# Kernel optimization log

Measured on AMD Instinct MI355X. Metric: run time of the kernel, lower is better.

Reference implementation:

```python
import jax, jax.numpy as jnp
import numpy as np

N, E, D = 100_000, 1_250_000, 64
EPS = 1e-8

def setup_inputs() -> dict:
    key = jax.random.key(0)
    ks = jax.random.split(key, 8)
    h = jax.random.normal(ks[0], (N, D), jnp.float32)
    eig = jax.random.normal(ks[1], (E, 1), jnp.float32)          # per-edge vector field
    snorm_n = jax.random.uniform(ks[2], (N, 1), jnp.float32)     # node norm
    src = jax.random.randint(ks[3], (E,), 0, N)
    dst = jax.random.randint(ks[4], (E,), 0, N)
    # pretrans: Linear(2D -> D); posttrans: Linear((3+1)*D -> D); torch Linear weight is [out, in]
    W1 = jax.random.normal(ks[5], (D, 2 * D), jnp.float32) / np.sqrt(2.0 * D)
    b1 = jnp.zeros((D,), jnp.float32)
    W2 = jax.random.normal(ks[6], (D, 4 * D), jnp.float32) / np.sqrt(4.0 * D)
    b2 = jnp.zeros((D,), jnp.float32)
    gamma = jnp.ones((D,), jnp.float32)   # BatchNorm1d weight
    beta = jnp.zeros((D,), jnp.float32)   # BatchNorm1d bias
    return dict(h=h, eig=eig, snorm_n=snorm_n, src=src, dst=dst,
                W1=W1, b1=b1, W2=W2, b2=b2, gamma=gamma, beta=beta)

def reference(h, eig, snorm_n, src, dst, W1, b1, W2, b2, gamma, beta):
    seg = lambda x: jax.ops.segment_sum(x, dst, num_segments=N)
    # pretrans on edges: MLP(cat[h_src, h_dst])
    z2 = jnp.concatenate([h[src], h[dst]], axis=1)   # [E, 2D]
    e = z2 @ W1.T + b1                                # [E, D]
    deg = seg(jnp.ones((E, 1), e.dtype))              # [N, 1]
    # aggregator: mean
    agg_mean = seg(e) / jnp.maximum(deg, 1.0)
    # aggregator: max (empty segments -> 0)
    agg_max = jax.ops.segment_max(e, dst, num_segments=N)
    agg_max = jnp.where(deg > 0, agg_max, 0.0)
    # aggregator: directional derivative dir_dx
    absum = seg(jnp.abs(eig))                         # [N, 1] sum of |vf| per node
    w = eig / (absum[dst] + EPS)                      # [E, 1] normalized weights
    agg_dir = jnp.abs(seg(e * w) - seg(w) * h)        # [N, D]
    # posttrans on nodes
    hc = jnp.concatenate([h, agg_mean, agg_max, agg_dir], axis=1)  # [N, 4D]
    h2 = (hc @ W2.T + b2) * snorm_n
    # BatchNorm1d (training mode: batch stats, biased variance)
    mu = jnp.mean(h2, axis=0)
    var = jnp.var(h2, axis=0)
    h2 = (h2 - mu) * jax.lax.rsqrt(var + 1e-5) * gamma + beta
    h2 = jax.nn.relu(h2)
    # residual (in_dim == out_dim); dropout p=0 is identity
    return h + h2
```

## Files before the change

### kernel.cpp

```cpp
#include <hip/hip_runtime.h>
#include <math.h>

__device__ __forceinline__ float bf2f(unsigned short s) {
    return __uint_as_float(((unsigned)s) << 16);
}
__device__ __forceinline__ unsigned short f2bf(float f) {
    unsigned u = __float_as_uint(f);
    unsigned r = (u + 0x7fffu + ((u >> 16) & 1u)) >> 16;
    return (unsigned short)r;
}

typedef __attribute__((ext_vector_type(8))) short short8v;
typedef __attribute__((ext_vector_type(4))) float f32x4;

__global__ __launch_bounds__(256) void edge_rank_kernel(
    const int* __restrict__ dst, int* __restrict__ cursor, int* __restrict__ rank, int E)
{
    int e = blockIdx.x * 256 + threadIdx.x;
    if (e < E) {
        rank[e] = atomicAdd(&cursor[dst[e]], 1);
    }
}

__global__ __launch_bounds__(256) void block_reduce_kernel(
    const int* __restrict__ deg, int* __restrict__ bsum, int N)
{
    __shared__ int sd[256];
    int t = threadIdx.x;
    int i = blockIdx.x * 256 + t;
    sd[t] = (i < N) ? deg[i] : 0;
    __syncthreads();
    for (int s = 128; s > 0; s >>= 1) {
        if (t < s) sd[t] += sd[t + s];
        __syncthreads();
    }
    if (t == 0) bsum[blockIdx.x] = sd[0];
}

__global__ __launch_bounds__(1024) void scan_bsums_kernel(
    const int* __restrict__ bsum, int* __restrict__ bscan, int nb)
{
    __shared__ int sd[1024];
    int t = threadIdx.x;
    int own = (t < nb) ? bsum[t] : 0;
    sd[t] = own;
    __syncthreads();
    for (int off = 1; off < 1024; off <<= 1) {
        int v = (t >= off) ? sd[t - off] : 0;
        __syncthreads();
        sd[t] += v;
        __syncthreads();
    }
    if (t < nb) bscan[t] = sd[t] - own;
}

__global__ __launch_bounds__(256) void block_scan_kernel(
    const int* __restrict__ deg, const int* __restrict__ bscan,
    int* __restrict__ offs, int N)
{
    __shared__ int sd[256];
    int t = threadIdx.x;
    int i = blockIdx.x * 256 + t;
    int myv = (i < N) ? deg[i] : 0;
    sd[t] = myv;
    __syncthreads();
    for (int off = 1; off < 256; off <<= 1) {
        int v = (t >= off) ? sd[t - off] : 0;
        __syncthreads();
        sd[t] += v;
        __syncthreads();
    }
    if (i < N) {
        offs[i] = sd[t] - myv + bscan[blockIdx.x];
    }
}

__global__ __launch_bounds__(256) void csr_scatter_kernel(
    const int* __restrict__ src, const int* __restrict__ dst, const float* __restrict__ eig,
    const int* __restrict__ rank, const int* __restrict__ offs,
    int2* __restrict__ csr, int E)
{
    int e = blockIdx.x * 256 + threadIdx.x;
    if (e < E) {
        int dn = dst[e];
        int p = offs[dn] + rank[e];
        csr[p] = make_int2(src[e], __float_as_int(eig[e]));
    }
}

__global__ __launch_bounds__(256) void uv_kernel(
    const float* __restrict__ h, const float* __restrict__ W1, const float* __restrict__ b1,
    unsigned short* __restrict__ u, unsigned short* __restrict__ v,
    unsigned short* __restrict__ hb, int N)
{
    __shared__ float wT[64 * 128];
    __shared__ float hs[64 * 68];
    int t = threadIdx.x;
    for (int idx = t; idx < 64 * 128; idx += 256) {
        int j = idx >> 7, c = idx & 127;
        int d = c & 63;
        int col = (c < 64) ? j : (64 + j);
        wT[idx] = W1[d * 128 + col];
    }
    int n0 = blockIdx.x * 64;
    for (int r = 0; r < 16; ++r) {
        int idx = r * 256 + t;
        int nl = idx >> 6, j = idx & 63;
        int n = n0 + nl;
        hs[nl * 68 + j] = (n < N) ? h[(size_t)n * 64 + j] : 0.f;
    }
    __syncthreads();

    for (int it = 0; it < 2; ++it) {
        int idx = it * 256 + t;
        int nl = idx >> 3, j8 = idx & 7;
        int n = n0 + nl;
        if (n < N) {
            union { unsigned short s[8]; uint4 v4; } pk;
#pragma unroll
            for (int m = 0; m < 8; ++m) pk.s[m] = f2bf(hs[nl * 68 + j8 * 8 + m]);
            *(uint4*)(hb + (size_t)n * 64 + j8 * 8) = pk.v4;
        }
    }

    int nb = (t & 15) * 4;
    int cb = (t >> 4) * 8;
    float acc[4][8];
#pragma unroll
    for (int i = 0; i < 4; ++i)
#pragma unroll
        for (int k = 0; k < 8; ++k) acc[i][k] = 0.f;

    for (int j = 0; j < 64; ++j) {
        float wv[8];
#pragma unroll
        for (int k = 0; k < 8; ++k) wv[k] = wT[j * 128 + cb + k];
#pragma unroll
        for (int i = 0; i < 4; ++i) {
            float hv = hs[(nb + i) * 68 + j];
#pragma unroll
            for (int k = 0; k < 8; ++k) acc[i][k] = fmaf(hv, wv[k], acc[i][k]);
        }
    }

    bool isV = (cb >= 64);
    int dbase = cb & 63;
#pragma unroll
    for (int i = 0; i < 4; ++i) {
        int n = n0 + nb + i;
        if (n < N) {
            union { unsigned short s[8]; uint4 v4; } pk;
            if (!isV) {
#pragma unroll
                for (int k = 0; k < 8; ++k) pk.s[k] = f2bf(acc[i][k]);
                *(uint4*)(u + (size_t)n * 64 + dbase) = pk.v4;
            } else {
#pragma unroll
                for (int k = 0; k < 8; ++k) pk.s[k] = f2bf(acc[i][k] + b1[dbase + k]);
                *(uint4*)(v + (size_t)n * 64 + dbase) = pk.v4;
            }
        }
    }
}

__global__ __launch_bounds__(256) void w2bf_kernel(
    const float* __restrict__ W2, unsigned short* __restrict__ w2bf)
{
    int idx = blockIdx.x * 256 + threadIdx.x;
    if (idx < 64 * 256) w2bf[idx] = f2bf(W2[idx]);
}

__global__ __launch_bounds__(256) void agg_kernel(
    const unsigned short* __restrict__ u, const unsigned short* __restrict__ v,
    const float* __restrict__ h,
    const int* __restrict__ offs, const int* __restrict__ degi,
    const int2* __restrict__ csr,
    unsigned short* __restrict__ agg, int N)
{
    int gw = (blockIdx.x * 256 + threadIdx.x) >> 6;
    int lane = threadIdx.x & 63;
    int n = __builtin_amdgcn_readfirstlane(gw);
    if (n >= N) return;
    int beg = offs[n];
    int dn = degi[n];

    float accs = 0.f, accd = 0.f, accm = -3.402823466e38f;
    float pa = 0.f, ps = 0.f;
    for (int i0 = 0; i0 < dn; i0 += 64) {
        int cnt = min(dn - i0, 64);
        int idxv = 0; float wvv = 0.f;
        if (lane < cnt) {
            int2 rec = csr[beg + i0 + lane];
            idxv = rec.x;
            wvv = __int_as_float(rec.y);
        }
        pa += fabsf(wvv);
        ps += wvv;
        int j = 0;
        for (; j + 4 <= cnt; j += 4) {
            int s0 = __shfl(idxv, j), s1 = __shfl(idxv, j + 1);
            int s2 = __shfl(idxv, j + 2), s3 = __shfl(idxv, j + 3);
            float w0 = __shfl(wvv, j), w1 = __shfl(wvv, j + 1);
            float w2_ = __shfl(wvv, j + 2), w3 = __shfl(wvv, j + 3);
            float u0 = bf2f(u[(size_t)s0 * 64 + lane]);
            float u1 = bf2f(u[(size_t)s1 * 64 + lane]);
            float u2 = bf2f(u[(size_t)s2 * 64 + lane]);
            float u3 = bf2f(u[(size_t)s3 * 64 + lane]);
            accs += (u0 + u1) + (u2 + u3);
            accm = fmaxf(accm, fmaxf(fmaxf(u0, u1), fmaxf(u2, u3)));
            accd = fmaf(w0, u0, fmaf(w1, u1, fmaf(w2_, u2, fmaf(w3, u3, accd))));
        }
        for (; j < cnt; ++j) {
            int s0 = __shfl(idxv, j);
            float w0 = __shfl(wvv, j);
            float u0 = bf2f(u[(size_t)s0 * 64 + lane]);
            accs += u0;
            accm = fmaxf(accm, u0);
            accd = fmaf(w0, u0, accd);
        }
    }
#pragma unroll
    for (int w = 1; w < 64; w <<= 1) {
        pa += __shfl_xor(pa, w);
        ps += __shfl_xor(ps, w);
    }
    float inv_ab = 1.f / (pa + 1e-8f);
    float segw = ps * inv_ab;

    float vl = bf2f(v[(size_t)n * 64 + lane]);
    float hl = h[(size_t)n * 64 + lane];
    float fdeg = (float)dn;
    float mean = (accs + fdeg * vl) / fmaxf(fdeg, 1.f);
    float amax = (dn > 0) ? (accm + vl) : 0.f;
    float adir = fabsf(fmaf(accd, inv_ab, segw * (vl - hl)));
    size_t base = (size_t)n * 192;
    agg[base + lane]       = f2bf(mean);
    agg[base + 64 + lane]  = f2bf(amax);
    agg[base + 128 + lane] = f2bf(adir);
}

__global__ __launch_bounds__(256) void post_mfma_kernel(
    const unsigned short* __restrict__ hb, const unsigned short* __restrict__ agg,
    const unsigned short* __restrict__ w2bf, const float* __restrict__ b2,
    const float* __restrict__ snorm, float* __restrict__ h2,
    float* __restrict__ bn_buf, int N)
{
    int lane = threadIdx.x & 63;
    int w = threadIdx.x >> 6;
    int lr = lane & 15;
    int lg = lane >> 4;

    short8v a[8];
    {
        const unsigned short* ab = w2bf + ((size_t)(w * 16 + lr)) * 256 + lg * 8;
#pragma unroll
        for (int s = 0; s < 8; ++s)
            a[s] = *(const short8v*)(ab + s * 32);
    }
    float4 b2v = *(const float4*)(b2 + w * 16 + lg * 4);
    float b2a[4] = {b2v.x, b2v.y, b2v.z, b2v.w};

    int n0 = blockIdx.x * 256;
    float s1[4] = {0.f, 0.f, 0.f, 0.f}, s2[4] = {0.f, 0.f, 0.f, 0.f};

#pragma unroll 2
    for (int t = 0; t < 16; ++t) {
        int node = n0 + t * 16 + lr;
        bool ok = node < N;
        short8v b[8];
        if (ok) {
            const unsigned short* hbp = hb  + (size_t)node * 64  + lg * 8;
            const unsigned short* agp = agg + (size_t)node * 192 + lg * 8;
            b[0] = *(const short8v*)(hbp);
            b[1] = *(const short8v*)(hbp + 32);
#pragma unroll
            for (int s = 2; s < 8; ++s)
                b[s] = *(const short8v*)(agp + (s - 2) * 32);
        } else {
#pragma unroll
            for (int s = 0; s < 8; ++s) b[s] = (short8v)0;
        }
        f32x4 acc0 = {0.f, 0.f, 0.f, 0.f}, acc1 = {0.f, 0.f, 0.f, 0.f};
#pragma unroll
        for (int s = 0; s < 8; s += 2) {
            acc0 = __builtin_amdgcn_mfma_f32_16x16x32_bf16(a[s],     b[s],     acc0, 0, 0, 0);
            acc1 = __builtin_amdgcn_mfma_f32_16x16x32_bf16(a[s + 1], b[s + 1], acc1, 0, 0, 0);
        }
        float sn = ok ? snorm[node] : 0.f;
        float xr[4];
#pragma unroll
        for (int r = 0; r < 4; ++r) {
            xr[r] = (acc0[r] + acc1[r] + b2a[r]) * sn;
            s1[r] += xr[r];
            s2[r] = fmaf(xr[r], xr[r], s2[r]);
        }
        if (ok) {
            *(float4*)(h2 + (size_t)node * 64 + w * 16 + lg * 4) =
                make_float4(xr[0], xr[1], xr[2], xr[3]);
        }
    }

#pragma unroll
    for (int m = 1; m < 16; m <<= 1) {
#pragma unroll
        for (int r = 0; r < 4; ++r) {
            s1[r] += __shfl_xor(s1[r], m);
            s2[r] += __shfl_xor(s2[r], m);
        }
    }
    if (lr == 0) {
        int d = w * 16 + lg * 4;
#pragma unroll
        for (int r = 0; r < 4; ++r) {
            atomicAdd(&bn_buf[d + r], s1[r]);
            atomicAdd(&bn_buf[64 + d + r], s2[r]);
        }
    }
}

__global__ __launch_bounds__(256) void bn_final_kernel(
    const float* __restrict__ h, const float* __restrict__ h2,
    const float* __restrict__ bn_buf, const float* __restrict__ gamma,
    const float* __restrict__ beta, float* __restrict__ out, int N, float invN)
{
    int idx = blockIdx.x * 256 + threadIdx.x;
    int total4 = N * 16;
    if (idx >= total4) return;
    int base = idx * 4;
    int d0 = base & 63;
    const float4 a = *(const float4*)(h2 + base);
    const float4 hh = *(const float4*)(h + base);
    float r[4] = {a.x, a.y, a.z, a.w};
    float hv[4] = {hh.x, hh.y, hh.z, hh.w};
    float o[4];
#pragma unroll
    for (int k = 0; k < 4; ++k) {
        int d = d0 + k;
        float mu = bn_buf[d] * invN;
        float var = bn_buf[64 + d] * invN - mu * mu;
        float rstd = rsqrtf(var + 1e-5f);
        float x = (r[k] - mu) * rstd * gamma[d] + beta[d];
        o[k] = hv[k] + fmaxf(x, 0.f);
    }
    float4 ov = {o[0], o[1], o[2], o[3]};
    *(float4*)(out + base) = ov;
}

extern "C" void kernel_launch(void* const* d_in, const int* in_sizes, int n_in,
                              void* d_out, int out_size, void* d_ws, size_t ws_size,
                              hipStream_t stream)
{
    const float* h     = (const float*)d_in[0];
    const float* eig   = (const float*)d_in[1];
    const float* snorm = (const float*)d_in[2];
    const int*   src   = (const int*)d_in[3];
    const int*   dst   = (const int*)d_in[4];
    const float* W1    = (const float*)d_in[5];
    const float* b1    = (const float*)d_in[6];
    const float* W2    = (const float*)d_in[7];
    const float* b2    = (const float*)d_in[8];
    const float* gamma = (const float*)d_in[9];
    const float* beta  = (const float*)d_in[10];
    float* out = (float*)d_out;

    const int N = in_sizes[2];
    const int E = in_sizes[1];

    char* w = (char*)d_ws;
    size_t off = 0;
    auto alloc = [&](size_t bytes) -> char* {
        char* p = w + off;
        off += (bytes + 255) & ~size_t(255);
        return p;
    };
    unsigned short* u = (unsigned short*)alloc((size_t)N * 64 * 2);
    unsigned short* v = (unsigned short*)alloc((size_t)N * 64 * 2);
    float* h2 = (float*)u;
    unsigned short* agg = (unsigned short*)alloc((size_t)N * 192 * 2);
    unsigned short* hb  = (unsigned short*)alloc((size_t)N * 64 * 2);
    int2* csr = (int2*)alloc((size_t)E * 8);
    int*  rank = (int*)alloc((size_t)E * 4);
    char* zero_base = w + off;
    int*   cursor = (int*)alloc((size_t)N * 4);
    float* bn_buf = (float*)alloc(128 * 4);
    size_t zero_bytes = (size_t)((char*)(bn_buf + 128) - zero_base);
    int* offs = (int*)alloc((size_t)N * 4);
    int nb = (N + 255) / 256;
    int* bsum  = (int*)alloc((size_t)nb * 4);
    int* bscan = (int*)alloc((size_t)nb * 4);
    unsigned short* w2bf = (unsigned short*)alloc(64 * 256 * 2);
    (void)ws_size; (void)n_in; (void)out_size;

    hipMemsetAsync(zero_base, 0, zero_bytes, stream);

    int egrid = (E + 255) / 256;
    edge_rank_kernel<<<egrid, 256, 0, stream>>>(dst, cursor, rank, E);
    block_reduce_kernel<<<nb, 256, 0, stream>>>(cursor, bsum, N);
    scan_bsums_kernel<<<1, 1024, 0, stream>>>(bsum, bscan, nb);
    block_scan_kernel<<<nb, 256, 0, stream>>>(cursor, bscan, offs, N);
    csr_scatter_kernel<<<egrid, 256, 0, stream>>>(src, dst, eig, rank, offs, csr, E);

    int ntiles = (N + 63) / 64;
    uv_kernel<<<ntiles, 256, 0, stream>>>(h, W1, b1, u, v, hb, N);
    w2bf_kernel<<<64, 256, 0, stream>>>(W2, w2bf);

    int agrid = ((size_t)N * 64 + 255) / 256;
    agg_kernel<<<agrid, 256, 0, stream>>>(u, v, h, offs, cursor, csr, agg, N);

    post_mfma_kernel<<<(N + 255) / 256, 256, 0, stream>>>(hb, agg, w2bf, b2, snorm,
                                                          h2, bn_buf, N);

    int fgrid = (N * 16 + 255) / 256;
    bn_final_kernel<<<fgrid, 256, 0, stream>>>(h, h2, bn_buf, gamma, beta, out, N, 1.0f / (float)N);
}
```

Measured before the change: 374.6 us.

## Move pretrans node projection to bf16 MFMA and shrink post-MLP tiles

The scalar FP32 shared-memory GEMM that computes per-node u/v projections is replaced by a bf16 MFMA kernel reading a pre-cast bf16 copy of h and a pre-transposed bf16 W1. The h cast and weight conversion move into separate elementwise kernels, and the W1/W2 conversions are merged into one launch. The post-MLP MFMA kernel now handles 64 nodes per block instead of 256, giving four times as many blocks for better occupancy. The trade-off is an extra launch and an extra pass over h, plus u/v computed from bf16-rounded h rather than fp32 h.

Result: slower. 435.1 us (+16.1%).

```diff
diff --git a/kernel.cpp b/kernel.cpp
--- a/kernel.cpp
+++ b/kernel.cpp
@@ -88,86 +88,94 @@
     }
 }
 
-__global__ __launch_bounds__(256) void uv_kernel(
-    const float* __restrict__ h, const float* __restrict__ W1, const float* __restrict__ b1,
-    unsigned short* __restrict__ u, unsigned short* __restrict__ v,
-    unsigned short* __restrict__ hb, int N)
-{
-    __shared__ float wT[64 * 128];
-    __shared__ float hs[64 * 68];
-    int t = threadIdx.x;
-    for (int idx = t; idx < 64 * 128; idx += 256) {
-        int j = idx >> 7, c = idx & 127;
-        int d = c & 63;
-        int col = (c < 64) ? j : (64 + j);
-        wT[idx] = W1[d * 128 + col];
-    }
+__global__ __launch_bounds__(256) void hb_cast_kernel(
+    const float* __restrict__ h, unsigned short* __restrict__ hb, long total8)
+{
+    long idx = (long)blockIdx.x * 256 + threadIdx.x;
+    if (idx >= total8) return;
+    const float4 a = *(const float4*)(h + idx * 8);
+    const float4 b = *(const float4*)(h + idx * 8 + 4);
+    union { unsigned short s[8]; uint4 v4; } pk;
+    pk.s[0] = f2bf(a.x); pk.s[1] = f2bf(a.y); pk.s[2] = f2bf(a.z); pk.s[3] = f2bf(a.w);
+    pk.s[4] = f2bf(b.x); pk.s[5] = f2bf(b.y); pk.s[6] = f2bf(b.z); pk.s[7] = f2bf(b.w);
+    *(uint4*)(hb + idx * 8) = pk.v4;
+}
+
+__global__ __launch_bounds__(256) void wprep_kernel(
+    const float* __restrict__ W1, const float* __restrict__ W2,
+    unsigned short* __restrict__ w1bf, unsigned short* __restrict__ w2bf)
+{
+    int idx = blockIdx.x * 256 + threadIdx.x;
+    if (idx < 128 * 64) {
+        int c = idx >> 6, j = idx & 63;
+        float val = (c < 64) ? W1[c * 128 + j] : W1[(c - 64) * 128 + 64 + j];
+        w1bf[idx] = f2bf(val);
+    } else if (idx < 128 * 64 + 64 * 256) {
+        int k = idx - 128 * 64;
+        w2bf[k] = f2bf(W2[k]);
+    }
+}
+
+__global__ __launch_bounds__(256) void uv_mfma_kernel(
+    const unsigned short* __restrict__ hb, const unsigned short* __restrict__ w1bf,
+    const float* __restrict__ b1,
+    unsigned short* __restrict__ u, unsigned short* __restrict__ v, int N)
+{
+    int lane = threadIdx.x & 63;
+    int wv = threadIdx.x >> 6;
+    int lr = lane & 15;
+    int lg = lane >> 4;
+
+    short8v a[2][2];
+#pragma unroll
+    for (int rt = 0; rt < 2; ++rt)
+#pragma unroll
+        for (int s = 0; s < 2; ++s)
+            a[rt][s] = *(const short8v*)(w1bf + (size_t)(wv * 32 + rt * 16 + lr) * 64 + s * 32 + lg * 8);
+
+    float b1v[2][4];
+#pragma unroll
+    for (int rt = 0; rt < 2; ++rt) {
+        if (wv >= 2) {
+            float4 t4 = *(const float4*)(b1 + (wv - 2) * 32 + rt * 16 + lg * 4);
+            b1v[rt][0] = t4.x; b1v[rt][1] = t4.y; b1v[rt][2] = t4.z; b1v[rt][3] = t4.w;
+        } else {
+            b1v[rt][0] = b1v[rt][1] = b1v[rt][2] = b1v[rt][3] = 0.f;
+        }
+    }
+
+    unsigned short* outp = (wv < 2) ? u : v;
+    int coff0 = (wv & 1) * 32 + lg * 4;
+
     int n0 = blockIdx.x * 64;
-    for (int r = 0; r < 16; ++r) {
-        int idx = r * 256 + t;
-        int nl = idx >> 6, j = idx & 63;
-        int n = n0 + nl;
-        hs[nl * 68 + j] = (n < N) ? h[(size_t)n * 64 + j] : 0.f;
-    }
-    __syncthreads();
-
-    for (int it = 0; it < 2; ++it) {
-        int idx = it * 256 + t;
-        int nl = idx >> 3, j8 = idx & 7;
-        int n = n0 + nl;
-        if (n < N) {
-            union { unsigned short s[8]; uint4 v4; } pk;
-#pragma unroll
-            for (int m = 0; m < 8; ++m) pk.s[m] = f2bf(hs[nl * 68 + j8 * 8 + m]);
-            *(uint4*)(hb + (size_t)n * 64 + j8 * 8) = pk.v4;
-        }
-    }
-
-    int nb = (t & 15) * 4;
-    int cb = (t >> 4) * 8;
-    float acc[4][8];
-#pragma unroll
-    for (int i = 0; i < 4; ++i)
-#pragma unroll
-        for (int k = 0; k < 8; ++k) acc[i][k] = 0.f;
-
-    for (int j = 0; j < 64; ++j) {
-        float wv[8];
-#pragma unroll
-        for (int k = 0; k < 8; ++k) wv[k] = wT[j * 128 + cb + k];
-#pragma unroll
-        for (int i = 0; i < 4; ++i) {
-            float hv = hs[(nb + i) * 68 + j];
-#pragma unroll
-            for (int k = 0; k < 8; ++k) acc[i][k] = fmaf(hv, wv[k], acc[i][k]);
-        }
-    }
-
-    bool isV = (cb >= 64);
-    int dbase = cb & 63;
-#pragma unroll
-    for (int i = 0; i < 4; ++i) {
-        int n = n0 + nb + i;
-        if (n < N) {
-            union { unsigned short s[8]; uint4 v4; } pk;
-            if (!isV) {
-#pragma unroll
-                for (int k = 0; k < 8; ++k) pk.s[k] = f2bf(acc[i][k]);
-                *(uint4*)(u + (size_t)n * 64 + dbase) = pk.v4;
-            } else {
-#pragma unroll
-                for (int k = 0; k < 8; ++k) pk.s[k] = f2bf(acc[i][k] + b1[dbase + k]);
-                *(uint4*)(v + (size_t)n * 64 + dbase) = pk.v4;
-            }
-        }
-    }
-}
-
-__global__ __launch_bounds__(256) void w2bf_kernel(
-    const float* __restrict__ W2, unsigned short* __restrict__ w2bf)
-{
-    int idx = blockIdx.x * 256 + threadIdx.x;
-    if (idx < 64 * 256) w2bf[idx] = f2bf(W2[idx]);
+#pragma unroll
+    for (int t = 0; t < 4; ++t) {
+        int node = n0 + t * 16 + lr;
+        bool ok = node < N;
+        short8v b[2];
+        if (ok) {
+            const unsigned short* hp = hb + (size_t)node * 64 + lg * 8;
+            b[0] = *(const short8v*)(hp);
+            b[1] = *(const short8v*)(hp + 32);
+        } else {
+            b[0] = (short8v)0; b[1] = (short8v)0;
+        }
+        f32x4 acc0 = {0.f, 0.f, 0.f, 0.f}, acc1 = {0.f, 0.f, 0.f, 0.f};
+#pragma unroll
+        for (int s = 0; s < 2; ++s) {
+            acc0 = __builtin_amdgcn_mfma_f32_16x16x32_bf16(a[0][s], b[s], acc0, 0, 0, 0);
+            acc1 = __builtin_amdgcn_mfma_f32_16x16x32_bf16(a[1][s], b[s], acc1, 0, 0, 0);
+        }
+        if (ok) {
+            union { unsigned short s[4]; uint2 v2; } pk;
+#pragma unroll
+            for (int r = 0; r < 4; ++r) pk.s[r] = f2bf(acc0[r] + b1v[0][r]);
+            *(uint2*)(outp + (size_t)node * 64 + coff0) = pk.v2;
+#pragma unroll
+            for (int r = 0; r < 4; ++r) pk.s[r] = f2bf(acc1[r] + b1v[1][r]);
+            *(uint2*)(outp + (size_t)node * 64 + coff0 + 16) = pk.v2;
+        }
+    }
 }
 
 __global__ __launch_bounds__(256) void agg_kernel(
@@ -260,11 +268,11 @@
     float4 b2v = *(const float4*)(b2 + w * 16 + lg * 4);
     float b2a[4] = {b2v.x, b2v.y, b2v.z, b2v.w};
 
-    int n0 = blockIdx.x * 256;
+    int n0 = blockIdx.x * 64;
     float s1[4] = {0.f, 0.f, 0.f, 0.f}, s2[4] = {0.f, 0.f, 0.f, 0.f};
 
 #pragma unroll 2
-    for (int t = 0; t < 16; ++t) {
+    for (int t = 0; t < 4; ++t) {
         int node = n0 + t * 16 + lr;
         bool ok = node < N;
         short8v b[8];
@@ -388,6 +396,7 @@
     int nb = (N + 255) / 256;
     int* bsum  = (int*)alloc((size_t)nb * 4);
     int* bscan = (int*)alloc((size_t)nb * 4);
+    unsigned short* w1bf = (unsigned short*)alloc(128 * 64 * 2);
     unsigned short* w2bf = (unsigned short*)alloc(64 * 256 * 2);
     (void)ws_size; (void)n_in; (void)out_size;
 
@@ -400,15 +409,18 @@
     block_scan_kernel<<<nb, 256, 0, stream>>>(cursor, bscan, offs, N);
     csr_scatter_kernel<<<egrid, 256, 0, stream>>>(src, dst, eig, rank, offs, csr, E);
 
-    int ntiles = (N + 63) / 64;
-    uv_kernel<<<ntiles, 256, 0, stream>>>(h, W1, b1, u, v, hb, N);
-    w2bf_kernel<<<64, 256, 0, stream>>>(W2, w2bf);
+    long total8 = (long)N * 8;
+    int hgrid = (int)((total8 + 255) / 256);
+    hb_cast_kernel<<<hgrid, 256, 0, stream>>>(h, hb, total8);
+    wprep_kernel<<<(128 * 64 + 64 * 256 + 255) / 256, 256, 0, stream>>>(W1, W2, w1bf, w2bf);
+
+    uv_mfma_kernel<<<(N + 63) / 64, 256, 0, stream>>>(hb, w1bf, b1, u, v, N);
 
     int agrid = ((size_t)N * 64 + 255) / 256;
     agg_kernel<<<agrid, 256, 0, stream>>>(u, v, h, offs, cursor, csr, agg, N);
 
-    post_mfma_kernel<<<(N + 255) / 256, 256, 0, stream>>>(hb, agg, w2bf, b2, snorm,
-                                                          h2, bn_buf, N);
+    post_mfma_kernel<<<(N + 63) / 64, 256, 0, stream>>>(hb, agg, w2bf, b2, snorm,
+                                                        h2, bn_buf, N);
 
     int fgrid = (N * 16 + 255) / 256;
     bn_final_kernel<<<fgrid, 256, 0, stream>>>(h, h2, bn_buf, gamma, beta, out, N, 1.0f / (float)N);
```
